# Kernel tuning notes

Measured on AMD Instinct MI355X. Metric: run time of the kernel, lower is better.

## Reference

```python
import jax, jax.numpy as jnp
import numpy as np

B, H, L, D = 2, 16, 2048, 128

def setup_inputs() -> dict:
    key = jax.random.key(0)
    kq, kk, kv = jax.random.split(key, 3)
    Q = jax.random.normal(kq, (B, H, L, D), dtype=jnp.float32)
    K = jax.random.normal(kk, (B, H, L, D), dtype=jnp.float32)
    V = jax.random.normal(kv, (B, H, L, D), dtype=jnp.float32)
    # causal mask: True where attention is allowed
    mask = jnp.broadcast_to(jnp.tril(jnp.ones((L, L), dtype=bool)), (B, H, L, L))
    return {"Q": Q, "K": K, "V": V, "mask": mask}

def reference(Q, K, V, mask):
    d_k = Q.shape[-1]
    scale = 1.0 / jnp.sqrt(jnp.asarray(d_k, dtype=Q.dtype))
    # [B,H,Lq,Lk] score matrix (naive materialization, as in the original)
    scores = jnp.einsum('bhqd,bhkd->bhqk', Q, K) * scale
    scores = jnp.where(mask, scores, -jnp.inf)
    attn = jax.nn.softmax(scores, axis=-1)
    return jnp.einsum('bhqk,bhkd->bhqd', attn, V)
```

## Files before the change

kernel.cpp:

```cpp
#include <hip/hip_runtime.h>
#include <hip/hip_bf16.h>

namespace {

constexpr int Bc = 2, Hc = 16, Lc = 2048, Dc = 128;
constexpr int KVBLK = 64;
constexpr int BH  = Bc * Hc;
constexpr int NKT = Lc / KVBLK;
constexpr int QB4 = 128;
constexpr int NQT4 = Lc / QB4;
constexpr float SCALE = 0.08838834764831845f * 1.4426950408889634f;

using f32x4   = __attribute__((ext_vector_type(4))) float;
using f32x16  = __attribute__((ext_vector_type(16))) float;
using short8  = __attribute__((ext_vector_type(8))) short;

union FragU { short8 v; short4 h[2]; };

__device__ inline short f2bf(float f) {
  unsigned u = __builtin_bit_cast(unsigned, f);
  u += 0x7fffu + ((u >> 16) & 1u);
  return (short)(u >> 16);
}

__device__ inline void gload_lds16(const short* g, short* l) {
  __builtin_amdgcn_global_load_lds(
      (const __attribute__((address_space(1))) void*)g,
      (__attribute__((address_space(3))) void*)l, 16, 0, 0);
}

__global__ __launch_bounds__(256) void conv_k(const float* __restrict__ Kg,
                                              short* __restrict__ Kw) {
  int tid = blockIdx.x * 256 + threadIdx.x;
  int x   = tid & 15;
  int row = (tid >> 4) & 63;
  int tb  = tid >> 10;
  int g   = x ^ (row & 7);
  int chunk = g >> 1, hi = g & 1;
  const float* src = Kg + ((size_t)tb * 64 + row) * 128 + chunk * 16 + hi * 4;
  float4 a = *(const float4*)src;
  float4 b = *(const float4*)(src + 8);
  short8 v;
  v[0] = f2bf(a.x); v[1] = f2bf(a.y); v[2] = f2bf(a.z); v[3] = f2bf(a.w);
  v[4] = f2bf(b.x); v[5] = f2bf(b.y); v[6] = f2bf(b.z); v[7] = f2bf(b.w);
  *(short8*)(Kw + (size_t)tb * 8192 + row * 128 + x * 8) = v;
}

__global__ __launch_bounds__(256) void conv_v(const float* __restrict__ Vg,
                                              short* __restrict__ Vw) {
  __shared__ short Vs[64 * 130];
  int tb  = blockIdx.x;
  int tid = threadIdx.x;
  const float* vt = Vg + (size_t)tb * 8192;
#pragma unroll
  for (int p = 0; p < 8; ++p) {
    int g  = p * 256 + tid;
    int kv = g >> 5;
    int c4 = g & 31;
    float4 v = *((const float4*)vt + g);
    short* d = &Vs[kv * 130 + c4 * 4];
    d[0] = f2bf(v.x); d[1] = f2bf(v.y); d[2] = f2bf(v.z); d[3] = f2bf(v.w);
  }
  __syncthreads();
#pragma unroll
  for (int p = 0; p < 4; ++p) {
    int gg = p * 256 + tid;
    int d  = gg >> 3;
    int x  = gg & 7;
    int g  = x ^ (d & 7);
    int chunk = g >> 1, hi = g & 1;
    int k0 = chunk * 16 + hi * 4;
    short8 o;
#pragma unroll
    for (int j = 0; j < 4; ++j) o[j]     = Vs[(k0 + j)     * 130 + d];
#pragma unroll
    for (int j = 0; j < 4; ++j) o[4 + j] = Vs[(k0 + 8 + j) * 130 + d];
    *(short8*)(Vw + (size_t)tb * 8192 + d * 64 + x * 8) = o;
  }
}

__global__ __launch_bounds__(256, 2) void attn_fwd4(
    const float* __restrict__ Qg, const short* __restrict__ Kw,
    const short* __restrict__ Vw, float* __restrict__ Og) {

  __shared__ __align__(16) short lds[2][2][8192];

  const int tid  = threadIdx.x;
  const int wave = tid >> 6;
  const int lane = tid & 63;
  const int hi   = lane >> 5;
  const int ln   = lane & 31;
  const int sw   = (ln & 7) << 4;

  const int bid = blockIdx.x;
  const int bh  = bid & (BH - 1);
  const int r5  = bid >> 5;
  const int qt  = (bid < 256) ? (NQT4 - 1 - r5) : (r5 - 8);
  const int q0w = qt * QB4 + wave * 32;

  const float* Qp  = Qg + (size_t)bh * Lc * Dc;
  float*       Op  = Og + (size_t)bh * Lc * Dc;
  const short* Kwp = Kw + (size_t)bh * NKT * 8192;
  const short* Vwp = Vw + (size_t)bh * NKT * 8192;

  short8 qf[8];
  {
    const float* qrow = Qp + (size_t)(q0w + ln) * Dc + hi * 4;
#pragma unroll
    for (int ks = 0; ks < 8; ++ks) {
      float4 a = *(const float4*)(qrow + ks * 16);
      float4 b = *(const float4*)(qrow + ks * 16 + 8);
      short8 v;
      v[0] = f2bf(a.x * SCALE); v[1] = f2bf(a.y * SCALE);
      v[2] = f2bf(a.z * SCALE); v[3] = f2bf(a.w * SCALE);
      v[4] = f2bf(b.x * SCALE); v[5] = f2bf(b.y * SCALE);
      v[6] = f2bf(b.z * SCALE); v[7] = f2bf(b.w * SCALE);
      qf[ks] = v;
    }
  }

  float m_run = -1e30f, l_run = 0.0f;
  f32x16 oacc[4];
#pragma unroll
  for (int nt = 0; nt < 4; ++nt)
#pragma unroll
    for (int r = 0; r < 16; ++r) oacc[nt][r] = 0.0f;

  const int ntiles = 2 * (qt + 1);

  auto stage = [&](int t, int b) {
    const short* gk = Kwp + (size_t)t * 8192 + tid * 8;
    const short* gv = Vwp + (size_t)t * 8192 + tid * 8;
    short* lk = &lds[b][0][tid * 8];
    short* lv = &lds[b][1][tid * 8];
#pragma unroll
    for (int i = 0; i < 4; ++i) gload_lds16(gk + i * 2048, lk + i * 2048);
#pragma unroll
    for (int i = 0; i < 4; ++i) gload_lds16(gv + i * 2048, lv + i * 2048);
  };

  stage(0, 0);

  for (int t = 0; t < ntiles; ++t) {
    const int cur = t & 1;
    __builtin_amdgcn_s_barrier();
    if (t + 1 < ntiles) {
      stage(t + 1, cur ^ 1);
      asm volatile("s_waitcnt vmcnt(8)" ::: "memory");
    } else {
      asm volatile("s_waitcnt vmcnt(0)" ::: "memory");
    }
    __builtin_amdgcn_s_barrier();
    __builtin_amdgcn_sched_barrier(0);

    const int kv0 = t * KVBLK;
    if (q0w + 31 < kv0) continue;

    const char* Kl = (const char*)&lds[cur][0][0];
    const char* Vl = (const char*)&lds[cur][1][0];

    f32x16 s0, s1;
#pragma unroll
    for (int r = 0; r < 16; ++r) { s0[r] = 0.0f; s1[r] = 0.0f; }
    __builtin_amdgcn_s_setprio(1);
#pragma unroll
    for (int ks = 0; ks < 8; ++ks) {
      FragU a0, a1;
      int col = (ks * 32 + hi * 16) ^ sw;
      a0.v = *(const short8*)(Kl + ln * 256        + col);
      a1.v = *(const short8*)(Kl + (32 + ln) * 256 + col);
      s0 = __builtin_amdgcn_mfma_f32_32x32x16_bf16(a0.v, qf[ks], s0, 0, 0, 0);
      s1 = __builtin_amdgcn_mfma_f32_32x32x16_bf16(a1.v, qf[ks], s1, 0, 0, 0);
    }
    __builtin_amdgcn_s_setprio(0);

    if (kv0 + 63 > q0w) {
      const int qg = q0w + ln;
#pragma unroll
      for (int r = 0; r < 16; ++r) {
        int kvr = kv0 + (r & 3) + 8 * (r >> 2) + 4 * hi;
        if (kvr > qg)      s0[r] = -1e30f;
        if (kvr + 32 > qg) s1[r] = -1e30f;
      }
    }

    float mx = s0[0];
#pragma unroll
    for (int r = 1; r < 16; ++r) mx = fmaxf(mx, s0[r]);
#pragma unroll
    for (int r = 0; r < 16; ++r) mx = fmaxf(mx, s1[r]);
    mx = fmaxf(mx, __shfl_xor(mx, 32));

    if (!__all(mx - m_run <= 8.0f)) {
      float mnew = fmaxf(m_run, mx);
      float corr = exp2f(m_run - mnew);
      m_run = mnew;
      l_run *= corr;
#pragma unroll
      for (int r = 0; r < 16; ++r) {
        int qrow = (r & 3) + 8 * (r >> 2) + 4 * hi;
        float c = __shfl(corr, qrow);
#pragma unroll
        for (int nt = 0; nt < 4; ++nt) oacc[nt][r] *= c;
      }
    }

    float rs = 0.0f;
    short8 pf[4];
#pragma unroll
    for (int kc = 0; kc < 4; ++kc) {
      short8 v;
#pragma unroll
      for (int e = 0; e < 8; ++e) {
        float sv = (kc < 2) ? s0[kc * 8 + e] : s1[(kc - 2) * 8 + e];
        float p = exp2f(sv - m_run);
        rs += p;
        v[e] = f2bf(p);
      }
      pf[kc] = v;
    }
    rs += __shfl_xor(rs, 32);
    l_run += rs;

    __builtin_amdgcn_s_setprio(1);
#pragma unroll
    for (int nt = 0; nt < 4; ++nt) {
      const char* vrow = Vl + (nt * 32 + ln) * 128;
#pragma unroll
      for (int kc = 0; kc < 4; ++kc) {
        FragU b;
        b.v = *(const short8*)(vrow + ((kc * 32 + hi * 16) ^ sw));
        oacc[nt] = __builtin_amdgcn_mfma_f32_32x32x16_bf16(pf[kc], b.v, oacc[nt], 0, 0, 0);
      }
    }
    __builtin_amdgcn_s_setprio(0);
  }

  float linv = 1.0f / l_run;
#pragma unroll
  for (int r = 0; r < 16; ++r) {
    int qrow = (r & 3) + 8 * (r >> 2) + 4 * hi;
    float il = __shfl(linv, qrow);
    float* orow = Op + (size_t)(q0w + qrow) * Dc + ln;
#pragma unroll
    for (int nt = 0; nt < 4; ++nt)
      orow[nt * 32] = oacc[nt][r] * il;
  }
}

__device__ inline unsigned packbf(float a, float b) {
  return (unsigned)(unsigned short)f2bf(a) | ((unsigned)(unsigned short)f2bf(b) << 16);
}

__global__ __launch_bounds__(256, 2) void attn_fb(
    const float* __restrict__ Qg, const float* __restrict__ Kg,
    const float* __restrict__ Vg, float* __restrict__ Og) {
  __shared__ __align__(16) short Klds[KVBLK * Dc];
  __shared__ __align__(16) short Vt[Dc * 68];
  const int tid = threadIdx.x, wave = tid >> 6, lane = tid & 63;
  const int lg = lane >> 4, lr = lane & 15;
  const int bid = blockIdx.x;
  const int bh = bid & (BH - 1);
  const int qt = 31 - (bid >> 5);
  const int q0w = qt * 64 + wave * 16;
  const float* Qp = Qg + (size_t)bh * Lc * Dc;
  const float* Kp = Kg + (size_t)bh * Lc * Dc;
  const float* Vp = Vg + (size_t)bh * Lc * Dc;
  float* Op = Og + (size_t)bh * Lc * Dc;
  short8 qf[4];
  {
    const float* qrow = Qp + (size_t)(q0w + lr) * Dc;
#pragma unroll
    for (int dc = 0; dc < 4; ++dc) {
      float4 a = *(const float4*)(qrow + dc * 32 + lg * 4);
      float4 b = *(const float4*)(qrow + dc * 32 + 16 + lg * 4);
      short8 v;
      v[0]=f2bf(a.x*SCALE); v[1]=f2bf(a.y*SCALE); v[2]=f2bf(a.z*SCALE); v[3]=f2bf(a.w*SCALE);
      v[4]=f2bf(b.x*SCALE); v[5]=f2bf(b.y*SCALE); v[6]=f2bf(b.z*SCALE); v[7]=f2bf(b.w*SCALE);
      qf[dc] = v;
    }
  }
  const f32x4 zero4 = {0.f,0.f,0.f,0.f};
  float m_run = -1e30f, l_run = 0.0f;
  f32x4 oacc[8];
#pragma unroll
  for (int dt = 0; dt < 8; ++dt) oacc[dt] = zero4;
  const int ntiles = qt + 1, c4 = tid & 31, rK = tid >> 5;
  for (int t = 0; t < ntiles; ++t) {
    const int kv0 = t * KVBLK;
    __syncthreads();
#pragma unroll
    for (int p = 0; p < 8; ++p) {
      int row = rK + p * 8;
      float4 k4 = *(const float4*)(Kp + (size_t)(kv0 + row) * Dc + c4 * 4);
      short4 pk; pk.x=f2bf(k4.x); pk.y=f2bf(k4.y); pk.z=f2bf(k4.z); pk.w=f2bf(k4.w);
      *(short4*)((char*)Klds + row * 256 + ((c4 * 8) ^ ((row & 7) << 4))) = pk;
    }
#pragma unroll
    for (int p = 0; p < 4; ++p) {
      int r0 = rK * 2 + p * 16;
      float4 v0 = *(const float4*)(Vp + (size_t)(kv0 + r0) * Dc + c4 * 4);
      float4 v1 = *(const float4*)(Vp + (size_t)(kv0 + r0 + 1) * Dc + c4 * 4);
      char* vb = (char*)Vt + r0 * 2;
      *(unsigned*)(vb + (c4*4+0)*136) = packbf(v0.x, v1.x);
      *(unsigned*)(vb + (c4*4+1)*136) = packbf(v0.y, v1.y);
      *(unsigned*)(vb + (c4*4+2)*136) = packbf(v0.z, v1.z);
      *(unsigned*)(vb + (c4*4+3)*136) = packbf(v0.w, v1.w);
    }
    __syncthreads();
    f32x4 st[4];
#pragma unroll
    for (int mt = 0; mt < 4; ++mt) st[mt] = zero4;
#pragma unroll
    for (int dc = 0; dc < 4; ++dc)
#pragma unroll
      for (int mt = 0; mt < 4; ++mt) {
        int row = mt * 16 + lr, sw2 = (row & 7) << 4;
        FragU a;
        a.h[0] = *(short4*)((char*)Klds + row*256 + ((dc*64      + lg*8) ^ sw2));
        a.h[1] = *(short4*)((char*)Klds + row*256 + ((dc*64 + 32 + lg*8) ^ sw2));
        st[mt] = __builtin_amdgcn_mfma_f32_16x16x32_bf16(a.v, qf[dc], st[mt], 0, 0, 0);
      }
    if (t == ntiles - 1) {
      const int qg = q0w + lr;
#pragma unroll
      for (int mt = 0; mt < 4; ++mt)
#pragma unroll
        for (int r = 0; r < 4; ++r)
          if (kv0 + mt * 16 + lg * 4 + r > qg) st[mt][r] = -1e30f;
    }
    float mx = st[0][0];
#pragma unroll
    for (int mt = 0; mt < 4; ++mt)
#pragma unroll
      for (int r = 0; r < 4; ++r) mx = fmaxf(mx, st[mt][r]);
    mx = fmaxf(mx, __shfl_xor(mx, 16));
    mx = fmaxf(mx, __shfl_xor(mx, 32));
    float mnew = fmaxf(m_run, mx);
    float corr = exp2f(m_run - mnew);
    m_run = mnew;
    float pr[4][4]; float rs = 0.0f;
#pragma unroll
    for (int mt = 0; mt < 4; ++mt)
#pragma unroll
      for (int r = 0; r < 4; ++r) { float e = exp2f(st[mt][r] - mnew); pr[mt][r] = e; rs += e; }
    rs += __shfl_xor(rs, 16);
    rs += __shfl_xor(rs, 32);
    l_run = l_run * corr + rs;
#pragma unroll
    for (int r = 0; r < 4; ++r) {
      float c = __shfl(corr, (lane & 48) + lg * 4 + r);
#pragma unroll
      for (int dt = 0; dt < 8; ++dt) oacc[dt][r] *= c;
    }
    short8 pf[2];
#pragma unroll
    for (int c = 0; c < 2; ++c) {
      short8 v;
      v[0]=f2bf(pr[2*c][0]); v[1]=f2bf(pr[2*c][1]); v[2]=f2bf(pr[2*c][2]); v[3]=f2bf(pr[2*c][3]);
      v[4]=f2bf(pr[2*c+1][0]); v[5]=f2bf(pr[2*c+1][1]); v[6]=f2bf(pr[2*c+1][2]); v[7]=f2bf(pr[2*c+1][3]);
      pf[c] = v;
    }
#pragma unroll
    for (int dt = 0; dt < 8; ++dt) {
      int rowb = (dt * 16 + lr) * 136;
#pragma unroll
      for (int c = 0; c < 2; ++c) {
        FragU b;
        b.h[0] = *(short4*)((char*)Vt + rowb + c*64      + lg*8);
        b.h[1] = *(short4*)((char*)Vt + rowb + c*64 + 32 + lg*8);
        oacc[dt] = __builtin_amdgcn_mfma_f32_16x16x32_bf16(pf[c], b.v, oacc[dt], 0, 0, 0);
      }
    }
  }
#pragma unroll
  for (int r = 0; r < 4; ++r) {
    float li = __shfl(l_run, (lane & 48) + lg * 4 + r);
    float inv = 1.0f / li;
    float* orow = Op + (size_t)(q0w + lg * 4 + r) * Dc;
#pragma unroll
    for (int dt = 0; dt < 8; ++dt) orow[dt * 16 + lr] = oacc[dt][r] * inv;
  }
}

}

extern "C" void kernel_launch(void* const* d_in, const int* in_sizes, int n_in,
                              void* d_out, int out_size, void* d_ws, size_t ws_size,
                              hipStream_t stream) {
  const float* Q = (const float*)d_in[0];
  const float* K = (const float*)d_in[1];
  const float* V = (const float*)d_in[2];
  float* O = (float*)d_out;
  const size_t elems = (size_t)BH * Lc * Dc;
  const size_t need  = 2 * elems * sizeof(short);
  if (ws_size >= need) {
    short* Kw = (short*)d_ws;
    short* Vw = Kw + elems;
    conv_k<<<dim3(4096), dim3(256), 0, stream>>>(K, Kw);
    conv_v<<<dim3(1024), dim3(256), 0, stream>>>(V, Vw);
    attn_fwd4<<<dim3(BH * NQT4), dim3(256), 0, stream>>>(Q, Kw, Vw, O);
  } else {
    attn_fb<<<dim3(BH * NKT), dim3(256), 0, stream>>>(Q, K, V, O);
  }
}
```

Measured before the change: 91.39 us.

## Software-pipeline QK of next tile with PV of previous tile; merge K/V conversion

The attention kernel is restructured so each iteration computes the QK^T scores for tile t while issuing the PV MFMAs for tile t-1, using probabilities kept in registers from the previous iteration. V gets a triple LDS buffer so the previous tile's V stays resident while the next one is prefetched, and a final PV step drains the pipeline. The intent is to hide the softmax VALU/exp work behind matrix-core work. Softmax also uses packed bf16 conversion via v_cvt_pk_bf16_f32 and split max/sum reductions, and the K and V conversion kernels are merged into one launch. The cost is higher LDS use (five 16 KB buffers per block) and more register pressure from carrying pf across iterations, which could hurt occupancy at two blocks per CU.

Result: slower. 95.11 us (+4.1%).

```diff
diff --git a/kernel.cpp b/kernel.cpp
--- a/kernel.cpp
+++ b/kernel.cpp
@@ -7,8 +7,8 @@
 constexpr int KVBLK = 64;
 constexpr int BH  = Bc * Hc;
 constexpr int NKT = Lc / KVBLK;
-constexpr int QB4 = 128;
-constexpr int NQT4 = Lc / QB4;
+constexpr int QB  = 128;
+constexpr int NQT = Lc / QB;
 constexpr float SCALE = 0.08838834764831845f * 1.4426950408889634f;
 
 using f32x4   = __attribute__((ext_vector_type(4))) float;
@@ -16,6 +16,7 @@
 using short8  = __attribute__((ext_vector_type(8))) short;
 
 union FragU { short8 v; short4 h[2]; };
+union PFU  { short8 v; unsigned u[4]; };
 
 __device__ inline short f2bf(float f) {
   unsigned u = __builtin_bit_cast(unsigned, f);
@@ -29,61 +30,64 @@
       (__attribute__((address_space(3))) void*)l, 16, 0, 0);
 }
 
-__global__ __launch_bounds__(256) void conv_k(const float* __restrict__ Kg,
-                                              short* __restrict__ Kw) {
-  int tid = blockIdx.x * 256 + threadIdx.x;
-  int x   = tid & 15;
-  int row = (tid >> 4) & 63;
-  int tb  = tid >> 10;
-  int g   = x ^ (row & 7);
-  int chunk = g >> 1, hi = g & 1;
-  const float* src = Kg + ((size_t)tb * 64 + row) * 128 + chunk * 16 + hi * 4;
-  float4 a = *(const float4*)src;
-  float4 b = *(const float4*)(src + 8);
-  short8 v;
-  v[0] = f2bf(a.x); v[1] = f2bf(a.y); v[2] = f2bf(a.z); v[3] = f2bf(a.w);
-  v[4] = f2bf(b.x); v[5] = f2bf(b.y); v[6] = f2bf(b.z); v[7] = f2bf(b.w);
-  *(short8*)(Kw + (size_t)tb * 8192 + row * 128 + x * 8) = v;
-}
-
-__global__ __launch_bounds__(256) void conv_v(const float* __restrict__ Vg,
-                                              short* __restrict__ Vw) {
+__global__ __launch_bounds__(256) void conv_kv(const float* __restrict__ Kg,
+                                               const float* __restrict__ Vg,
+                                               short* __restrict__ Kw,
+                                               short* __restrict__ Vw) {
   __shared__ short Vs[64 * 130];
-  int tb  = blockIdx.x;
-  int tid = threadIdx.x;
-  const float* vt = Vg + (size_t)tb * 8192;
-#pragma unroll
-  for (int p = 0; p < 8; ++p) {
-    int g  = p * 256 + tid;
-    int kv = g >> 5;
-    int c4 = g & 31;
-    float4 v = *((const float4*)vt + g);
-    short* d = &Vs[kv * 130 + c4 * 4];
-    d[0] = f2bf(v.x); d[1] = f2bf(v.y); d[2] = f2bf(v.z); d[3] = f2bf(v.w);
-  }
-  __syncthreads();
-#pragma unroll
-  for (int p = 0; p < 4; ++p) {
-    int gg = p * 256 + tid;
-    int d  = gg >> 3;
-    int x  = gg & 7;
-    int g  = x ^ (d & 7);
+  const int b = blockIdx.x;
+  if (b < 4096) {
+    int tid = b * 256 + threadIdx.x;
+    int x   = tid & 15;
+    int row = (tid >> 4) & 63;
+    int tb  = tid >> 10;
+    int g   = x ^ (row & 7);
     int chunk = g >> 1, hi = g & 1;
-    int k0 = chunk * 16 + hi * 4;
-    short8 o;
-#pragma unroll
-    for (int j = 0; j < 4; ++j) o[j]     = Vs[(k0 + j)     * 130 + d];
-#pragma unroll
-    for (int j = 0; j < 4; ++j) o[4 + j] = Vs[(k0 + 8 + j) * 130 + d];
-    *(short8*)(Vw + (size_t)tb * 8192 + d * 64 + x * 8) = o;
-  }
-}
-
-__global__ __launch_bounds__(256, 2) void attn_fwd4(
+    const float* src = Kg + ((size_t)tb * 64 + row) * 128 + chunk * 16 + hi * 4;
+    float4 a = *(const float4*)src;
+    float4 c = *(const float4*)(src + 8);
+    short8 v;
+    v[0] = f2bf(a.x); v[1] = f2bf(a.y); v[2] = f2bf(a.z); v[3] = f2bf(a.w);
+    v[4] = f2bf(c.x); v[5] = f2bf(c.y); v[6] = f2bf(c.z); v[7] = f2bf(c.w);
+    *(short8*)(Kw + (size_t)tb * 8192 + row * 128 + x * 8) = v;
+  } else {
+    int tb  = b - 4096;
+    int tid = threadIdx.x;
+    const float* vt = Vg + (size_t)tb * 8192;
+#pragma unroll
+    for (int p = 0; p < 8; ++p) {
+      int g  = p * 256 + tid;
+      int kv = g >> 5;
+      int c4 = g & 31;
+      float4 v = *((const float4*)vt + g);
+      short* d = &Vs[kv * 130 + c4 * 4];
+      d[0] = f2bf(v.x); d[1] = f2bf(v.y); d[2] = f2bf(v.z); d[3] = f2bf(v.w);
+    }
+    __syncthreads();
+#pragma unroll
+    for (int p = 0; p < 4; ++p) {
+      int gg = p * 256 + tid;
+      int d  = gg >> 3;
+      int x  = gg & 7;
+      int g  = x ^ (d & 7);
+      int chunk = g >> 1, hi = g & 1;
+      int k0 = chunk * 16 + hi * 4;
+      short8 o;
+#pragma unroll
+      for (int j = 0; j < 4; ++j) o[j]     = Vs[(k0 + j)     * 130 + d];
+#pragma unroll
+      for (int j = 0; j < 4; ++j) o[4 + j] = Vs[(k0 + 8 + j) * 130 + d];
+      *(short8*)(Vw + (size_t)tb * 8192 + d * 64 + x * 8) = o;
+    }
+  }
+}
+
+__global__ __launch_bounds__(256, 2) void attn_fwd5(
     const float* __restrict__ Qg, const short* __restrict__ Kw,
     const short* __restrict__ Vw, float* __restrict__ Og) {
 
-  __shared__ __align__(16) short lds[2][2][8192];
+  __shared__ __align__(16) short K2[2][8192];
+  __shared__ __align__(16) short V3[3][8192];
 
   const int tid  = threadIdx.x;
   const int wave = tid >> 6;
@@ -95,8 +99,8 @@
   const int bid = blockIdx.x;
   const int bh  = bid & (BH - 1);
   const int r5  = bid >> 5;
-  const int qt  = (bid < 256) ? (NQT4 - 1 - r5) : (r5 - 8);
-  const int q0w = qt * QB4 + wave * 32;
+  const int qt  = (bid < 256) ? (NQT - 1 - r5) : (r5 - 8);
+  const int q0w = qt * QB + wave * 32;
 
   const float* Qp  = Qg + (size_t)bh * Lc * Dc;
   float*       Op  = Og + (size_t)bh * Lc * Dc;
@@ -127,25 +131,28 @@
     for (int r = 0; r < 16; ++r) oacc[nt][r] = 0.0f;
 
   const int ntiles = 2 * (qt + 1);
-
-  auto stage = [&](int t, int b) {
+  const int tlast  = min(ntiles - 1, (q0w + 31) >> 6);
+
+  auto stage = [&](int t, int kb, int vb) {
     const short* gk = Kwp + (size_t)t * 8192 + tid * 8;
     const short* gv = Vwp + (size_t)t * 8192 + tid * 8;
-    short* lk = &lds[b][0][tid * 8];
-    short* lv = &lds[b][1][tid * 8];
+    short* lk = &K2[kb][tid * 8];
+    short* lv = &V3[vb][tid * 8];
 #pragma unroll
     for (int i = 0; i < 4; ++i) gload_lds16(gk + i * 2048, lk + i * 2048);
 #pragma unroll
     for (int i = 0; i < 4; ++i) gload_lds16(gv + i * 2048, lv + i * 2048);
   };
 
-  stage(0, 0);
+  stage(0, 0, 0);
+  int vb_prev = 2, vb_cur = 0, vb_next = 1;
+  PFU pf[4];
 
   for (int t = 0; t < ntiles; ++t) {
     const int cur = t & 1;
     __builtin_amdgcn_s_barrier();
     if (t + 1 < ntiles) {
-      stage(t + 1, cur ^ 1);
+      stage(t + 1, cur ^ 1, vb_next);
       asm volatile("s_waitcnt vmcnt(8)" ::: "memory");
     } else {
       asm volatile("s_waitcnt vmcnt(0)" ::: "memory");
@@ -153,76 +160,101 @@
     __builtin_amdgcn_s_barrier();
     __builtin_amdgcn_sched_barrier(0);
 
+    const bool do_t = (t <= tlast);
+    const bool do_pv = (t >= 1) && (t - 1 <= tlast);
     const int kv0 = t * KVBLK;
-    if (q0w + 31 < kv0) continue;
-
-    const char* Kl = (const char*)&lds[cur][0][0];
-    const char* Vl = (const char*)&lds[cur][1][0];
 
     f32x16 s0, s1;
-#pragma unroll
-    for (int r = 0; r < 16; ++r) { s0[r] = 0.0f; s1[r] = 0.0f; }
-    __builtin_amdgcn_s_setprio(1);
-#pragma unroll
-    for (int ks = 0; ks < 8; ++ks) {
-      FragU a0, a1;
-      int col = (ks * 32 + hi * 16) ^ sw;
-      a0.v = *(const short8*)(Kl + ln * 256        + col);
-      a1.v = *(const short8*)(Kl + (32 + ln) * 256 + col);
-      s0 = __builtin_amdgcn_mfma_f32_32x32x16_bf16(a0.v, qf[ks], s0, 0, 0, 0);
-      s1 = __builtin_amdgcn_mfma_f32_32x32x16_bf16(a1.v, qf[ks], s1, 0, 0, 0);
-    }
-    __builtin_amdgcn_s_setprio(0);
-
-    if (kv0 + 63 > q0w) {
-      const int qg = q0w + ln;
-#pragma unroll
-      for (int r = 0; r < 16; ++r) {
-        int kvr = kv0 + (r & 3) + 8 * (r >> 2) + 4 * hi;
-        if (kvr > qg)      s0[r] = -1e30f;
-        if (kvr + 32 > qg) s1[r] = -1e30f;
-      }
-    }
-
-    float mx = s0[0];
-#pragma unroll
-    for (int r = 1; r < 16; ++r) mx = fmaxf(mx, s0[r]);
-#pragma unroll
-    for (int r = 0; r < 16; ++r) mx = fmaxf(mx, s1[r]);
-    mx = fmaxf(mx, __shfl_xor(mx, 32));
-
-    if (!__all(mx - m_run <= 8.0f)) {
-      float mnew = fmaxf(m_run, mx);
-      float corr = exp2f(m_run - mnew);
-      m_run = mnew;
-      l_run *= corr;
-#pragma unroll
-      for (int r = 0; r < 16; ++r) {
-        int qrow = (r & 3) + 8 * (r >> 2) + 4 * hi;
-        float c = __shfl(corr, qrow);
-#pragma unroll
-        for (int nt = 0; nt < 4; ++nt) oacc[nt][r] *= c;
-      }
-    }
-
-    float rs = 0.0f;
-    short8 pf[4];
-#pragma unroll
-    for (int kc = 0; kc < 4; ++kc) {
-      short8 v;
-#pragma unroll
-      for (int e = 0; e < 8; ++e) {
-        float sv = (kc < 2) ? s0[kc * 8 + e] : s1[(kc - 2) * 8 + e];
-        float p = exp2f(sv - m_run);
-        rs += p;
-        v[e] = f2bf(p);
-      }
-      pf[kc] = v;
-    }
-    rs += __shfl_xor(rs, 32);
-    l_run += rs;
-
-    __builtin_amdgcn_s_setprio(1);
+    if (do_t) {
+      const char* Kl = (const char*)&K2[cur][0];
+#pragma unroll
+      for (int r = 0; r < 16; ++r) { s0[r] = 0.0f; s1[r] = 0.0f; }
+      __builtin_amdgcn_s_setprio(1);
+#pragma unroll
+      for (int ks = 0; ks < 8; ++ks) {
+        FragU a0, a1;
+        int col = (ks * 32 + hi * 16) ^ sw;
+        a0.v = *(const short8*)(Kl + ln * 256        + col);
+        a1.v = *(const short8*)(Kl + (32 + ln) * 256 + col);
+        s0 = __builtin_amdgcn_mfma_f32_32x32x16_bf16(a0.v, qf[ks], s0, 0, 0, 0);
+        s1 = __builtin_amdgcn_mfma_f32_32x32x16_bf16(a1.v, qf[ks], s1, 0, 0, 0);
+      }
+      __builtin_amdgcn_s_setprio(0);
+    }
+
+    if (do_pv) {
+      const char* Vl = (const char*)&V3[vb_prev][0];
+      __builtin_amdgcn_s_setprio(1);
+#pragma unroll
+      for (int nt = 0; nt < 4; ++nt) {
+        const char* vrow = Vl + (nt * 32 + ln) * 128;
+#pragma unroll
+        for (int kc = 0; kc < 4; ++kc) {
+          FragU b;
+          b.v = *(const short8*)(vrow + ((kc * 32 + hi * 16) ^ sw));
+          oacc[nt] = __builtin_amdgcn_mfma_f32_32x32x16_bf16(pf[kc].v, b.v, oacc[nt], 0, 0, 0);
+        }
+      }
+      __builtin_amdgcn_s_setprio(0);
+    }
+
+    if (do_t) {
+      if (kv0 + 63 > q0w) {
+        const int qg = q0w + ln;
+#pragma unroll
+        for (int r = 0; r < 16; ++r) {
+          int kvr = kv0 + (r & 3) + 8 * (r >> 2) + 4 * hi;
+          if (kvr > qg)      s0[r] = -1e30f;
+          if (kvr + 32 > qg) s1[r] = -1e30f;
+        }
+      }
+      float ma = s0[0], mb = s0[8], mc = s1[0], md = s1[8];
+#pragma unroll
+      for (int r = 1; r < 8; ++r) {
+        ma = fmaxf(ma, s0[r]); mb = fmaxf(mb, s0[8 + r]);
+        mc = fmaxf(mc, s1[r]); md = fmaxf(md, s1[8 + r]);
+      }
+      float mx = fmaxf(fmaxf(ma, mb), fmaxf(mc, md));
+      mx = fmaxf(mx, __shfl_xor(mx, 32));
+
+      if (!__all(mx - m_run <= 8.0f)) {
+        float mnew = fmaxf(m_run, mx);
+        float corr = exp2f(m_run - mnew);
+        m_run = mnew;
+        l_run *= corr;
+#pragma unroll
+        for (int r = 0; r < 16; ++r) {
+          int qrow = (r & 3) + 8 * (r >> 2) + 4 * hi;
+          float c = __shfl(corr, qrow);
+#pragma unroll
+          for (int nt = 0; nt < 4; ++nt) oacc[nt][r] *= c;
+        }
+      }
+
+      float rsp[4] = {0.f, 0.f, 0.f, 0.f};
+#pragma unroll
+      for (int kc = 0; kc < 4; ++kc) {
+#pragma unroll
+        for (int w = 0; w < 4; ++w) {
+          int e = kc * 8 + w * 2;
+          float v0 = (kc < 2) ? (float)s0[e]     : (float)s1[e - 16];
+          float v1 = (kc < 2) ? (float)s0[e + 1] : (float)s1[e - 15];
+          float e0 = exp2f(v0 - m_run);
+          float e1 = exp2f(v1 - m_run);
+          rsp[w] += e0 + e1;
+          asm("v_cvt_pk_bf16_f32 %0, %1, %2" : "=v"(pf[kc].u[w]) : "v"(e0), "v"(e1));
+        }
+      }
+      float rs = (rsp[0] + rsp[1]) + (rsp[2] + rsp[3]);
+      rs += __shfl_xor(rs, 32);
+      l_run += rs;
+    }
+
+    int tmp = vb_prev; vb_prev = vb_cur; vb_cur = vb_next; vb_next = tmp;
+  }
+
+  if (tlast == ntiles - 1) {
+    const char* Vl = (const char*)&V3[vb_prev][0];
 #pragma unroll
     for (int nt = 0; nt < 4; ++nt) {
       const char* vrow = Vl + (nt * 32 + ln) * 128;
@@ -230,10 +262,9 @@
       for (int kc = 0; kc < 4; ++kc) {
         FragU b;
         b.v = *(const short8*)(vrow + ((kc * 32 + hi * 16) ^ sw));
-        oacc[nt] = __builtin_amdgcn_mfma_f32_32x32x16_bf16(pf[kc], b.v, oacc[nt], 0, 0, 0);
-      }
-    }
-    __builtin_amdgcn_s_setprio(0);
+        oacc[nt] = __builtin_amdgcn_mfma_f32_32x32x16_bf16(pf[kc].v, b.v, oacc[nt], 0, 0, 0);
+      }
+    }
   }
 
   float linv = 1.0f / l_run;
@@ -353,13 +384,13 @@
 #pragma unroll
       for (int dt = 0; dt < 8; ++dt) oacc[dt][r] *= c;
     }
-    short8 pf[2];
+    short8 pf2[2];
 #pragma unroll
     for (int c = 0; c < 2; ++c) {
       short8 v;
       v[0]=f2bf(pr[2*c][0]); v[1]=f2bf(pr[2*c][1]); v[2]=f2bf(pr[2*c][2]); v[3]=f2bf(pr[2*c][3]);
       v[4]=f2bf(pr[2*c+1][0]); v[5]=f2bf(pr[2*c+1][1]); v[6]=f2bf(pr[2*c+1][2]); v[7]=f2bf(pr[2*c+1][3]);
-      pf[c] = v;
+      pf2[c] = v;
     }
 #pragma unroll
     for (int dt = 0; dt < 8; ++dt) {
@@ -369,7 +400,7 @@
         FragU b;
         b.h[0] = *(short4*)((char*)Vt + rowb + c*64      + lg*8);
         b.h[1] = *(short4*)((char*)Vt + rowb + c*64 + 32 + lg*8);
-        oacc[dt] = __builtin_amdgcn_mfma_f32_16x16x32_bf16(pf[c], b.v, oacc[dt], 0, 0, 0);
+        oacc[dt] = __builtin_amdgcn_mfma_f32_16x16x32_bf16(pf2[c], b.v, oacc[dt], 0, 0, 0);
       }
     }
   }
@@ -397,9 +428,8 @@
   if (ws_size >= need) {
     short* Kw = (short*)d_ws;
     short* Vw = Kw + elems;
-    conv_k<<<dim3(4096), dim3(256), 0, stream>>>(K, Kw);
-    conv_v<<<dim3(1024), dim3(256), 0, stream>>>(V, Vw);
-    attn_fwd4<<<dim3(BH * NQT4), dim3(256), 0, stream>>>(Q, Kw, Vw, O);
+    conv_kv<<<dim3(4096 + 1024), dim3(256), 0, stream>>>(K, V, Kw, Vw);
+    attn_fwd5<<<dim3(BH * NQT), dim3(256), 0, stream>>>(Q, Kw, Vw, O);
   } else {
     attn_fb<<<dim3(BH * NKT), dim3(256), 0, stream>>>(Q, K, V, O);
   }
```
